# Performance work log

Measured on AMD Instinct MI355X. Metric: run time of the kernel, lower is better.

The kernel has to match this reference:

```python
import jax, jax.numpy as jnp
import numpy as np

B, T, D, E, L, MAXP, PRED, TOPK = 128, 2048, 256, 32, 8, 168, 168, 2
INIT_STD = 0.02


def setup_inputs() -> dict:
    key = jax.random.key(0)
    ks = jax.random.split(key, 18)
    n = jax.random.normal
    s = INIT_STD
    inp = {
        "ctx_embed": n(ks[0], (B, T, D), jnp.float32),
        "query_experts": n(ks[1], (E, MAXP, D), jnp.float32) * s,
        "query_pos": n(ks[2], (MAXP, D), jnp.float32) * s,
        "len_emb": n(ks[3], (MAXP + 1, D), jnp.float32),  # nn.Embedding table
        "latents": n(ks[4], (L, D), jnp.float32) * s,
        "w_lat_q": n(ks[5], (D, D), jnp.float32) / np.sqrt(D),
        "w_ctx_k": n(ks[6], (D, D), jnp.float32) / np.sqrt(D),
        "w_ctx_v": n(ks[7], (D, D), jnp.float32) / np.sqrt(D),
        "w_lat_out": n(ks[8], (D, D), jnp.float32) / np.sqrt(D),
        "w_step_q": n(ks[9], (D, D), jnp.float32) / np.sqrt(D),
        "w_lat_k": n(ks[10], (D, D), jnp.float32) / np.sqrt(D),
        "w_lat_v": n(ks[11], (D, D), jnp.float32) / np.sqrt(D),
        "w_step_out": n(ks[12], (D, D), jnp.float32) / np.sqrt(D),
        "gate_w1": n(ks[13], (2 * D, D), jnp.float32) / np.sqrt(2 * D),
        "gate_b1": jnp.zeros((D,), jnp.float32),
        "gate_w2": n(ks[14], (D, E), jnp.float32) / np.sqrt(D),
        "gate_b2": jnp.zeros((E,), jnp.float32),
        "pred_len": PRED,
    }
    return inp


def _sdpa_1head(q, k, v):
    # q: [B,Q,D], k/v: [B,K,D]; single-head scaled dot-product attention
    scale = jnp.asarray(q.shape[-1], q.dtype) ** -0.5
    attn = jax.nn.softmax(jnp.einsum('bqd,bkd->bqk', q, k) * scale, axis=-1)
    return jnp.einsum('bqk,bkd->bqd', attn, v)


def reference(ctx_embed, query_experts, query_pos, len_emb, latents,
              w_lat_q, w_ctx_k, w_ctx_v, w_lat_out,
              w_step_q, w_lat_k, w_lat_v, w_step_out,
              gate_w1, gate_b1, gate_w2, gate_b2, pred_len):
    Bb, Tt, Dd = ctx_embed.shape
    P = pred_len

    # step base: positional queries + pred-length embedding
    pos = query_pos[:P][None]                      # [1,P,D]
    len_vec = len_emb[P][None, None]               # [1,1,D]
    step_base = jnp.broadcast_to(pos + len_vec, (Bb, P, Dd))

    # latent <- context cross-attention
    lat = jnp.broadcast_to(latents[None], (Bb, latents.shape[0], Dd))
    q1 = lat @ w_lat_q
    k1 = ctx_embed @ w_ctx_k
    v1 = ctx_embed @ w_ctx_v
    lat_ctx = _sdpa_1head(q1, k1, v1) @ w_lat_out  # [B,L,D]

    # step <- latent cross-attention
    q2 = step_base @ w_step_q
    k2 = lat_ctx @ w_lat_k
    v2 = lat_ctx @ w_lat_v
    step_ctx = _sdpa_1head(q2, k2, v2) @ w_step_out  # [B,P,D]

    # gating MLP over [step_base, step_ctx]
    gate_inp = jnp.concatenate([step_base, step_ctx], axis=-1)  # [B,P,2D]
    h = jax.nn.gelu(gate_inp @ gate_w1 + gate_b1, approximate=False)
    logits = h @ gate_w2 + gate_b2                               # [B,P,E]

    # top-k masking + softmax (keep top-k logits, others -> -inf)
    topv = jax.lax.top_k(logits, TOPK)[0]
    kth = topv[..., -1:]
    masked = jnp.where(logits >= kth, logits, -jnp.inf)
    weights = jax.nn.softmax(masked, axis=-1)                    # [B,P,E]

    # mixture of expert queries (einsum avoids [B,P,E,D] intermediate)
    queries = jnp.einsum('bpe,epd->bpd', weights, query_experts[:, :P, :])
    return queries
```

## Files before the change

### kernel.cpp

```cpp
#include <hip/hip_runtime.h>
#include <math.h>

#define NB 128
#define NT 2048
#define ND 256
#define NE 32
#define NL 8
#define NP 168
#define SCL 0.0625f

#define OFF_QK   0
#define OFF_LATQ 2048
#define OFF_WVO  4096
#define OFF_WSO1 69632
#define OFF_WVW  135168
#define OFF_G0   200704
#define OFF_Q2S  243712
#define OFF_AV   286720
#define OFF_DEN  2383872
#define OFF_K2   2392064
#define OFF_VW   2654208

typedef __attribute__((ext_vector_type(8))) short short8b;
typedef __attribute__((ext_vector_type(4))) float f32x4;

static __device__ __forceinline__ unsigned short f2bf(float f){
  unsigned u = __float_as_uint(f);
  u += 0x7fffu + ((u >> 16) & 1u);
  return (unsigned short)(u >> 16);
}

static __device__ __forceinline__ short8b pack8(float4 lo, float4 hi){
  short8b r;
  r[0]=(short)f2bf(lo.x); r[1]=(short)f2bf(lo.y); r[2]=(short)f2bf(lo.z); r[3]=(short)f2bf(lo.w);
  r[4]=(short)f2bf(hi.x); r[5]=(short)f2bf(hi.y); r[6]=(short)f2bf(hi.z); r[7]=(short)f2bf(hi.w);
  return r;
}

__global__ __launch_bounds__(256) void pre1(const float* __restrict__ latents,
    const float* __restrict__ wlq, const float* __restrict__ wcv,
    const float* __restrict__ wlo, const float* __restrict__ wso,
    const float* __restrict__ gw1, const float* __restrict__ gb1,
    const float* __restrict__ qpos, const float* __restrict__ lemb,
    const float* __restrict__ wsq, float* __restrict__ ws)
{
  int bid = blockIdx.x, tid = threadIdx.x;
  if (bid < 256){
    const float* a = wcv + bid*ND;
    float acc = 0.f;
    #pragma unroll 8
    for (int k=0;k<ND;k++) acc += a[k]*wlo[k*ND+tid];
    ws[OFF_WVO + bid*ND + tid] = acc;
  } else if (bid < 512){
    int i = bid-256;
    const float* a = wso + i*ND;
    float acc = 0.f;
    #pragma unroll 8
    for (int k=0;k<ND;k++) acc += a[k]*gw1[(ND+k)*ND+tid];
    ws[OFF_WSO1 + i*ND + tid] = acc;
  } else if (bid < 512+NP){
    int p = bid-512;
    float ag = gb1[tid], aq = 0.f;
    #pragma unroll 4
    for (int j=0;j<ND;j++){
      float sb = qpos[p*ND+j] + lemb[NP*ND+j];
      ag += sb*gw1[j*ND+tid];
      aq += sb*wsq[j*ND+tid];
    }
    ws[OFF_G0  + p*ND + tid] = ag;
    ws[OFF_Q2S + p*ND + tid] = aq*SCL;
  } else {
    int l = bid-(512+NP);
    float acc = 0.f;
    #pragma unroll 8
    for (int m=0;m<ND;m++) acc += latents[l*ND+m]*wlq[m*ND+tid];
    ws[OFF_LATQ + l*ND + tid] = acc;
  }
}

__global__ __launch_bounds__(256) void pre2(const float* __restrict__ wck,
                                            const float* __restrict__ wlv,
                                            float* __restrict__ ws)
{
  int bid = blockIdx.x, tid = threadIdx.x;
  if (bid < 256){
    int d = bid;
    float wk = wck[d*ND + tid];
    float part[NL];
    #pragma unroll
    for (int l=0;l<NL;l++) part[l] = ws[OFF_LATQ + l*ND + tid]*wk;
    #pragma unroll
    for (int m=1;m<64;m<<=1){
      #pragma unroll
      for (int l=0;l<NL;l++) part[l] += __shfl_xor(part[l], m);
    }
    __shared__ float red[4][NL];
    if ((tid&63)==0){
      #pragma unroll
      for (int l=0;l<NL;l++) red[tid>>6][l] = part[l];
    }
    __syncthreads();
    if (tid < NL){
      float s = red[0][tid]+red[1][tid]+red[2][tid]+red[3][tid];
      ws[OFF_QK + tid*ND + d] = s*SCL;
    }
  } else {
    int dd = bid - 256;
    const float* a = wlv + dd*ND;
    float acc = 0.f;
    #pragma unroll 8
    for (int k=0;k<ND;k++) acc += a[k]*ws[OFF_WSO1 + k*ND + tid];
    ws[OFF_WVW + dd*ND + tid] = acc;
  }
}

__global__ __launch_bounds__(256,1) void kA(const float* __restrict__ ctx, float* __restrict__ ws)
{
  __shared__ float buf[2][64*256];
  __shared__ float efull[256*8];

  int bid = blockIdx.x;
  int b = bid >> 3, sp = bid & 7;
  int tid = threadIdx.x;
  int wv = tid >> 6, lane = tid & 63;
  int c = lane & 15, g = lane >> 4;
  int dq = lane;
  const int T0 = sp*256;

  short8b afrag[8];
  if (c < NL){
    const float* qk = ws + OFF_QK + c*ND + g*8;
    #pragma unroll
    for (int kk=0;kk<8;kk++){
      float4 lo = *(const float4*)(qk + kk*32);
      float4 hi = *(const float4*)(qk + kk*32 + 4);
      afrag[kk] = pack8(lo, hi);
    }
  } else {
    short8b z;
    #pragma unroll
    for (int j=0;j<8;j++) z[j] = 0;
    #pragma unroll
    for (int kk=0;kk<8;kk++) afrag[kk] = z;
  }

  float av[8][4];
  #pragma unroll
  for (int l=0;l<8;l++){
    #pragma unroll
    for (int j=0;j<4;j++) av[l][j] = 0.f;
  }

  int rr = wv*16 + c, r7 = rr & 7;

  int lofs[8];
  #pragma unroll
  for (int j=0;j<8;j++) lofs[j] = (lane ^ j) << 2;

  const float* g0 = ctx + ((size_t)(b*NT + T0 + wv*16))*ND;

#define STAGE(PBUF, GPTR) do{                                                     \
    _Pragma("unroll")                                                             \
    for (int i_=0;i_<16;i_++){                                                    \
      __builtin_amdgcn_global_load_lds(                                           \
          (const __attribute__((address_space(1))) void*)((GPTR) + i_*ND + lofs[i_&7]), \
          (__attribute__((address_space(3))) void*)((PBUF) + (wv*16+i_)*256), 16, 0, 0); \
    }                                                                             \
  }while(0)

  float* pc = &buf[0][0];
  float* pn = &buf[1][0];
  STAGE(pc, g0);

  #pragma unroll 1
  for (int sub=0; sub<4; ++sub){
    asm volatile("s_waitcnt lgkmcnt(0)" ::: "memory");
    __builtin_amdgcn_sched_barrier(0);
    if (sub < 3){
      STAGE(pn, g0 + (size_t)(sub+1)*64*ND);
      asm volatile("s_waitcnt vmcnt(16)" ::: "memory");
    } else {
      asm volatile("s_waitcnt vmcnt(0)" ::: "memory");
    }
    __builtin_amdgcn_sched_barrier(0);

    f32x4 acc = {0.f,0.f,0.f,0.f};
    #pragma unroll
    for (int kk=0;kk<8;kk++){
      int sA = 2*g + 8*kk;
      float4 lo = *(const float4*)(pc + rr*256 + (((sA  ) ^ r7)<<2));
      float4 hi = *(const float4*)(pc + rr*256 + (((sA+1) ^ r7)<<2));
      acc = __builtin_amdgcn_mfma_f32_16x16x32_bf16(afrag[kk], pack8(lo,hi), acc, 0, 0, 0);
    }
    if (g < 2){
      float4 ev = make_float4(__expf(acc[0]),__expf(acc[1]),__expf(acc[2]),__expf(acc[3]));
      *(float4*)&efull[(sub*64 + rr)*8 + g*4] = ev;
    }
    asm volatile("s_waitcnt lgkmcnt(0)" ::: "memory");
    __builtin_amdgcn_sched_barrier(0);

    #pragma unroll
    for (int i=0;i<16;i++){
      int tl = wv*16 + i;
      float4 c4 = *(const float4*)(pc + tl*256 + ((dq ^ (tl&7))<<2));
      const float* ep = efull + (sub*64 + tl)*8;
      float4 e0 = *(const float4*)ep;
      float4 e1 = *(const float4*)(ep+4);
      float e8[8];
      e8[0]=e0.x; e8[1]=e0.y; e8[2]=e0.z; e8[3]=e0.w;
      e8[4]=e1.x; e8[5]=e1.y; e8[6]=e1.z; e8[7]=e1.w;
      #pragma unroll
      for (int l=0;l<8;l++){
        av[l][0] += e8[l]*c4.x;
        av[l][1] += e8[l]*c4.y;
        av[l][2] += e8[l]*c4.z;
        av[l][3] += e8[l]*c4.w;
      }
    }
    float* t_ = pc; pc = pn; pn = t_;
  }
#undef STAGE

  __syncthreads();

  float* red = &buf[0][0];
  #pragma unroll
  for (int l=0;l<8;l++)
    *(float4*)(red + (((l*4 + wv)*64 + dq)<<2)) = make_float4(av[l][0],av[l][1],av[l][2],av[l][3]);

  if (wv == 0){
    float dpart[8];
    #pragma unroll
    for (int l=0;l<8;l++) dpart[l] = 0.f;
    #pragma unroll
    for (int q=0;q<4;q++){
      const float* ep = efull + (q*64 + lane)*8;
      float4 e0 = *(const float4*)ep;
      float4 e1 = *(const float4*)(ep+4);
      dpart[0]+=e0.x; dpart[1]+=e0.y; dpart[2]+=e0.z; dpart[3]+=e0.w;
      dpart[4]+=e1.x; dpart[5]+=e1.y; dpart[6]+=e1.z; dpart[7]+=e1.w;
    }
    #pragma unroll
    for (int m=1;m<64;m<<=1){
      #pragma unroll
      for (int l=0;l<8;l++) dpart[l] += __shfl_xor(dpart[l], m);
    }
    if (lane == 0){
      #pragma unroll
      for (int l=0;l<8;l++) ws[OFF_DEN + bid*8 + l] = dpart[l];
    }
  }
  __syncthreads();

  #pragma unroll
  for (int rep=0; rep<2; ++rep){
    int lidx = tid + rep*256;
    int l = lidx >> 6, d2 = lidx & 63;
    float4 s0 = *(const float4*)(red + (((l*4 + 0)*64 + d2)<<2));
    float4 s1 = *(const float4*)(red + (((l*4 + 1)*64 + d2)<<2));
    float4 s2 = *(const float4*)(red + (((l*4 + 2)*64 + d2)<<2));
    float4 s3 = *(const float4*)(red + (((l*4 + 3)*64 + d2)<<2));
    float4 o;
    o.x = s0.x+s1.x+s2.x+s3.x;
    o.y = s0.y+s1.y+s2.y+s3.y;
    o.z = s0.z+s1.z+s2.z+s3.z;
    o.w = s0.w+s1.w+s2.w+s3.w;
    *(float4*)&ws[OFF_AV + ((size_t)(bid*8 + l))*ND + d2*4] = o;
  }
}

__global__ __launch_bounds__(256) void kB1(const float* __restrict__ wlk,
                                           float* __restrict__ ws)
{
  int bid = blockIdx.x;
  int b = bid >> 1, half = bid & 1;
  int d = threadIdx.x;
  __shared__ float avnT[256][8];
  __shared__ float latT[256][8];

  float dent[8];
  #pragma unroll
  for (int l=0;l<8;l++){
    float s = 0.f;
    #pragma unroll
    for (int sp=0;sp<8;sp++) s += ws[OFF_DEN + (b*8+sp)*8 + l];
    dent[l] = s;
  }
  float av8[8];
  #pragma unroll
  for (int l=0;l<8;l++){
    float s = 0.f;
    #pragma unroll
    for (int sp=0;sp<8;sp++) s += ws[OFF_AV + ((size_t)((b*8+sp)*8 + l))*ND + d];
    av8[l] = s / dent[l];
  }
  *(float4*)&avnT[d][0] = make_float4(av8[0],av8[1],av8[2],av8[3]);
  *(float4*)&avnT[d][4] = make_float4(av8[4],av8[5],av8[6],av8[7]);
  __syncthreads();

  float lc[8];
  #pragma unroll
  for (int l=0;l<8;l++) lc[l] = 0.f;
  #pragma unroll 8
  for (int dd=0;dd<ND;dd++){
    float w = ws[OFF_WVO + dd*ND + d];
    float4 a0 = *(const float4*)&avnT[dd][0];
    float4 a1 = *(const float4*)&avnT[dd][4];
    lc[0]+=a0.x*w; lc[1]+=a0.y*w; lc[2]+=a0.z*w; lc[3]+=a0.w*w;
    lc[4]+=a1.x*w; lc[5]+=a1.y*w; lc[6]+=a1.z*w; lc[7]+=a1.w*w;
  }
  *(float4*)&latT[d][0] = make_float4(lc[0],lc[1],lc[2],lc[3]);
  *(float4*)&latT[d][4] = make_float4(lc[4],lc[5],lc[6],lc[7]);
  __syncthreads();

  const float* w3 = half ? (ws + OFF_WVW) : wlk;
  float o8[8];
  #pragma unroll
  for (int l=0;l<8;l++) o8[l] = 0.f;
  #pragma unroll 8
  for (int dd=0;dd<ND;dd++){
    float w = w3[dd*ND + d];
    float4 a0 = *(const float4*)&latT[dd][0];
    float4 a1 = *(const float4*)&latT[dd][4];
    o8[0]+=a0.x*w; o8[1]+=a0.y*w; o8[2]+=a0.z*w; o8[3]+=a0.w*w;
    o8[4]+=a1.x*w; o8[5]+=a1.y*w; o8[6]+=a1.z*w; o8[7]+=a1.w*w;
  }
  size_t obase = (half ? OFF_VW : OFF_K2) + (size_t)b*8*ND + d;
  #pragma unroll
  for (int l=0;l<8;l++) ws[obase + l*ND] = o8[l];
}

__global__ __launch_bounds__(256) void kB2(const float* __restrict__ ws,
    const float* __restrict__ gw2, const float* __restrict__ gb2,
    const float* __restrict__ qe, float* __restrict__ out)
{
  int bid = blockIdx.x;
  int b = bid / 6, p0 = (bid % 6)*28;
  int tid = threadIdx.x;

  __shared__ float q2h[28][260];
  __shared__ float k2s[8][260];
  __shared__ float vws[8][260];
  __shared__ float wexp[28][8];
  __shared__ float lg[28][33];
  __shared__ float4 sel[28];

  #pragma unroll
  for (int i=0;i<7;i++){
    int idx = tid + i*256;
    int r = idx >> 6, c4 = idx & 63;
    *(float4*)&q2h[r][c4*4] = *(const float4*)&ws[OFF_Q2S + (p0+r)*ND + c4*4];
  }
  #pragma unroll
  for (int i=0;i<2;i++){
    int idx = tid + i*256;
    int l = idx >> 6, c4 = idx & 63;
    *(float4*)&k2s[l][c4*4] = *(const float4*)&ws[OFF_K2 + (b*8+l)*ND + c4*4];
    *(float4*)&vws[l][c4*4] = *(const float4*)&ws[OFF_VW + (b*8+l)*ND + c4*4];
  }
  __syncthreads();

  {
    int pp = tid >> 3, l1 = tid & 7;
    if (pp < 28){
      float s2 = 0.f;
      #pragma unroll 8
      for (int i=0;i<64;i++){
        float4 qa = *(const float4*)&q2h[pp][4*i];
        float4 kb = *(const float4*)&k2s[l1][4*i];
        s2 += qa.x*kb.x + qa.y*kb.y + qa.z*kb.z + qa.w*kb.w;
      }
      float e2 = __expf(s2);
      float den = e2;
      den += __shfl_xor(den,1); den += __shfl_xor(den,2); den += __shfl_xor(den,4);
      wexp[pp][l1] = e2/den;
    }
  }
  __syncthreads();

  {
    float vcol[8];
    #pragma unroll
    for (int l=0;l<8;l++) vcol[l] = vws[l][tid];
    #pragma unroll 4
    for (int p=0;p<28;p++){
      float4 w0 = *(const float4*)&wexp[p][0];
      float4 w1v = *(const float4*)&wexp[p][4];
      float x = ws[OFF_G0 + (p0+p)*ND + tid]
              + w0.x*vcol[0]+w0.y*vcol[1]+w0.z*vcol[2]+w0.w*vcol[3]
              + w1v.x*vcol[4]+w1v.y*vcol[5]+w1v.z*vcol[6]+w1v.w*vcol[7];
      q2h[p][tid] = 0.5f*x*(1.f+erff(x*0.70710678118654752f));
    }
  }
  __syncthreads();

  {
    int e = tid & 31, pq = tid >> 5;
    if (pq < 7){
      float b2v = gb2[e];
      float a0=b2v, a1=b2v, a2=b2v, a3=b2v;
      for (int cc=0;cc<ND;cc+=4){
        float w20 = gw2[(cc+0)*NE + e];
        float w21 = gw2[(cc+1)*NE + e];
        float w22 = gw2[(cc+2)*NE + e];
        float w23 = gw2[(cc+3)*NE + e];
        float4 h0 = *(const float4*)&q2h[pq*4+0][cc];
        float4 h1 = *(const float4*)&q2h[pq*4+1][cc];
        float4 h2 = *(const float4*)&q2h[pq*4+2][cc];
        float4 h3 = *(const float4*)&q2h[pq*4+3][cc];
        a0 += h0.x*w20 + h0.y*w21 + h0.z*w22 + h0.w*w23;
        a1 += h1.x*w20 + h1.y*w21 + h1.z*w22 + h1.w*w23;
        a2 += h2.x*w20 + h2.y*w21 + h2.z*w22 + h2.w*w23;
        a3 += h3.x*w20 + h3.y*w21 + h3.z*w22 + h3.w*w23;
      }
      lg[pq*4+0][e] = a0;
      lg[pq*4+1][e] = a1;
      lg[pq*4+2][e] = a2;
      lg[pq*4+3][e] = a3;
    }
  }
  __syncthreads();

  if (tid < 28){
    float m1 = -1e30f, m2 = -1e30f;
    int e1 = 0, ee2 = 0;
    for (int e3=0;e3<NE;e3++){
      float v = lg[tid][e3];
      if (v > m1){ m2 = m1; ee2 = e1; m1 = v; e1 = e3; }
      else if (v > m2){ m2 = v; ee2 = e3; }
    }
    float z = __expf(m2 - m1);
    float inv = 1.f/(1.f+z);
    sel[tid] = make_float4(__int_as_float(e1), __int_as_float(ee2), inv, z*inv);
  }
  __syncthreads();

  for (int p=0;p<28;p++){
    float4 s = sel[p];
    int e1 = __float_as_int(s.x), ee2 = __float_as_int(s.y);
    float q1v = qe[((size_t)e1*NP + (p0+p))*ND + tid];
    float q2v = qe[((size_t)ee2*NP + (p0+p))*ND + tid];
    out[((size_t)b*NP + (p0+p))*ND + tid] = s.z*q1v + s.w*q2v;
  }
}

extern "C" void kernel_launch(void* const* d_in, const int* in_sizes, int n_in,
                              void* d_out, int out_size, void* d_ws, size_t ws_size,
                              hipStream_t stream)
{
  const float* ctx  = (const float*)d_in[0];
  const float* qe   = (const float*)d_in[1];
  const float* qpos = (const float*)d_in[2];
  const float* lemb = (const float*)d_in[3];
  const float* lat  = (const float*)d_in[4];
  const float* wlq  = (const float*)d_in[5];
  const float* wck  = (const float*)d_in[6];
  const float* wcv  = (const float*)d_in[7];
  const float* wlo  = (const float*)d_in[8];
  const float* wsq  = (const float*)d_in[9];
  const float* wlk  = (const float*)d_in[10];
  const float* wlv  = (const float*)d_in[11];
  const float* wso  = (const float*)d_in[12];
  const float* gw1  = (const float*)d_in[13];
  const float* gb1  = (const float*)d_in[14];
  const float* gw2  = (const float*)d_in[15];
  const float* gb2  = (const float*)d_in[16];
  float* out = (float*)d_out;
  float* ws  = (float*)d_ws;

  pre1<<<512+NP+NL, 256, 0, stream>>>(lat, wlq, wcv, wlo, wso, gw1, gb1, qpos, lemb, wsq, ws);
  pre2<<<512, 256, 0, stream>>>(wck, wlv, ws);
  kA  <<<NB*8, 256, 0, stream>>>(ctx, ws);
  kB1 <<<NB*2, 256, 0, stream>>>(wlk, ws);
  kB2 <<<NB*6, 256, 0, stream>>>(ws, gw2, gb2, qe, out);
}
```

Before: 164.2 us.

## Merge precompute kernels and make context-attention blocks persistent over many tiles

The two weight-precompute kernels become one launch. Each block recomputes its intermediate products locally, either through a shared-memory temporary or by reassociating the latent-query/key product, so pre2 no longer waits on pre1. The context-attention kernel now launches 256 persistent blocks, each streaming 16 tiles of 64 rows with double buffering. It writes per-wave partial attention sums and denominators instead of reducing in shared memory across waves. kB1 merges its two halves into one block per batch that sums 32 partials each, which cuts launches and block startup cost but enlarges the workspace partial traffic and halves parallelism in kB1.

```diff
diff --git a/kernel.cpp b/kernel.cpp
--- a/kernel.cpp
+++ b/kernel.cpp
@@ -10,16 +10,14 @@
 #define SCL 0.0625f
 
 #define OFF_QK   0
-#define OFF_LATQ 2048
 #define OFF_WVO  4096
-#define OFF_WSO1 69632
-#define OFF_WVW  135168
-#define OFF_G0   200704
-#define OFF_Q2S  243712
-#define OFF_AV   286720
-#define OFF_DEN  2383872
-#define OFF_K2   2392064
-#define OFF_VW   2654208
+#define OFF_WVW  69632
+#define OFF_G0   135168
+#define OFF_Q2S  178176
+#define OFF_AV   221184
+#define OFF_DEN  8609792
+#define OFF_K2   8642560
+#define OFF_VW   8904704
 
 typedef __attribute__((ext_vector_type(8))) short short8b;
 typedef __attribute__((ext_vector_type(4))) float f32x4;
@@ -37,9 +35,10 @@
   return r;
 }
 
-__global__ __launch_bounds__(256) void pre1(const float* __restrict__ latents,
-    const float* __restrict__ wlq, const float* __restrict__ wcv,
-    const float* __restrict__ wlo, const float* __restrict__ wso,
+__global__ __launch_bounds__(256) void preA(const float* __restrict__ latents,
+    const float* __restrict__ wlq, const float* __restrict__ wck,
+    const float* __restrict__ wcv, const float* __restrict__ wlo,
+    const float* __restrict__ wlv, const float* __restrict__ wso,
     const float* __restrict__ gw1, const float* __restrict__ gb1,
     const float* __restrict__ qpos, const float* __restrict__ lemb,
     const float* __restrict__ wsq, float* __restrict__ ws)
@@ -51,15 +50,8 @@
     #pragma unroll 8
     for (int k=0;k<ND;k++) acc += a[k]*wlo[k*ND+tid];
     ws[OFF_WVO + bid*ND + tid] = acc;
-  } else if (bid < 512){
-    int i = bid-256;
-    const float* a = wso + i*ND;
-    float acc = 0.f;
-    #pragma unroll 8
-    for (int k=0;k<ND;k++) acc += a[k]*gw1[(ND+k)*ND+tid];
-    ws[OFF_WSO1 + i*ND + tid] = acc;
-  } else if (bid < 512+NP){
-    int p = bid-512;
+  } else if (bid < 256+NP){
+    int p = bid-256;
     float ag = gb1[tid], aq = 0.f;
     #pragma unroll 4
     for (int j=0;j<ND;j++){
@@ -69,32 +61,28 @@
     }
     ws[OFF_G0  + p*ND + tid] = ag;
     ws[OFF_Q2S + p*ND + tid] = aq*SCL;
-  } else {
-    int l = bid-(512+NP);
-    float acc = 0.f;
+  } else if (bid < 256+NP+256){
+    int d = bid-(256+NP);
+    __shared__ float ck[ND];
+    __shared__ float red[4][NL];
+    ck[tid] = wck[d*ND + tid];
+    __syncthreads();
+    const float* wrow = wlq + tid*ND;
+    float macc = 0.f;
     #pragma unroll 8
-    for (int m=0;m<ND;m++) acc += latents[l*ND+m]*wlq[m*ND+tid];
-    ws[OFF_LATQ + l*ND + tid] = acc;
-  }
-}
-
-__global__ __launch_bounds__(256) void pre2(const float* __restrict__ wck,
-                                            const float* __restrict__ wlv,
-                                            float* __restrict__ ws)
-{
-  int bid = blockIdx.x, tid = threadIdx.x;
-  if (bid < 256){
-    int d = bid;
-    float wk = wck[d*ND + tid];
+    for (int k4=0;k4<64;k4++){
+      float4 w4 = *(const float4*)(wrow + k4*4);
+      float4 c4 = *(const float4*)(ck + k4*4);
+      macc += w4.x*c4.x + w4.y*c4.y + w4.z*c4.z + w4.w*c4.w;
+    }
     float part[NL];
     #pragma unroll
-    for (int l=0;l<NL;l++) part[l] = ws[OFF_LATQ + l*ND + tid]*wk;
+    for (int l=0;l<NL;l++) part[l] = latents[l*ND + tid]*macc;
     #pragma unroll
     for (int m=1;m<64;m<<=1){
       #pragma unroll
       for (int l=0;l<NL;l++) part[l] += __shfl_xor(part[l], m);
     }
-    __shared__ float red[4][NL];
     if ((tid&63)==0){
       #pragma unroll
       for (int l=0;l<NL;l++) red[tid>>6][l] = part[l];
@@ -105,11 +93,18 @@
       ws[OFF_QK + tid*ND + d] = s*SCL;
     }
   } else {
-    int dd = bid - 256;
+    int dd = bid-(256+NP+256);
+    __shared__ float tmp[ND];
     const float* a = wlv + dd*ND;
+    float t = 0.f;
+    #pragma unroll 8
+    for (int k=0;k<ND;k++) t += a[k]*wso[k*ND+tid];
+    tmp[tid] = t;
+    __syncthreads();
+    const float* gw1b = gw1 + (size_t)ND*ND;
     float acc = 0.f;
     #pragma unroll 8
-    for (int k=0;k<ND;k++) acc += a[k]*ws[OFF_WSO1 + k*ND + tid];
+    for (int m=0;m<ND;m++) acc += tmp[m]*gw1b[m*ND+tid];
     ws[OFF_WVW + dd*ND + tid] = acc;
   }
 }
@@ -120,12 +115,11 @@
   __shared__ float efull[256*8];
 
   int bid = blockIdx.x;
-  int b = bid >> 3, sp = bid & 7;
   int tid = threadIdx.x;
   int wv = tid >> 6, lane = tid & 63;
   int c = lane & 15, g = lane >> 4;
   int dq = lane;
-  const int T0 = sp*256;
+  int rr = wv*16 + c, r7 = rr & 7;
 
   short8b afrag[8];
   if (c < NL){
@@ -145,19 +139,19 @@
   }
 
   float av[8][4];
+  float den8[8];
   #pragma unroll
   for (int l=0;l<8;l++){
+    den8[l] = 0.f;
     #pragma unroll
     for (int j=0;j<4;j++) av[l][j] = 0.f;
   }
 
-  int rr = wv*16 + c, r7 = rr & 7;
-
   int lofs[8];
   #pragma unroll
   for (int j=0;j<8;j++) lofs[j] = (lane ^ j) << 2;
 
-  const float* g0 = ctx + ((size_t)(b*NT + T0 + wv*16))*ND;
+  const float* gw = ctx + ((size_t)bid*1024 + wv*16)*ND;
 
 #define STAGE(PBUF, GPTR) do{                                                     \
     _Pragma("unroll")                                                             \
@@ -168,16 +162,17 @@
     }                                                                             \
   }while(0)
 
-  float* pc = &buf[0][0];
-  float* pn = &buf[1][0];
-  STAGE(pc, g0);
+  STAGE(&buf[0][0], gw);
 
   #pragma unroll 1
-  for (int sub=0; sub<4; ++sub){
+  for (int s=0; s<16; ++s){
+    float* pc = &buf[s&1][0];
+    float* pn = &buf[(s&1)^1][0];
+    int sub = s & 3;
     asm volatile("s_waitcnt lgkmcnt(0)" ::: "memory");
     __builtin_amdgcn_sched_barrier(0);
-    if (sub < 3){
-      STAGE(pn, g0 + (size_t)(sub+1)*64*ND);
+    if (s < 15){
+      STAGE(pn, gw + (size_t)(s+1)*64*ND);
       asm volatile("s_waitcnt vmcnt(16)" ::: "memory");
     } else {
       asm volatile("s_waitcnt vmcnt(0)" ::: "memory");
@@ -215,85 +210,60 @@
         av[l][1] += e8[l]*c4.y;
         av[l][2] += e8[l]*c4.z;
         av[l][3] += e8[l]*c4.w;
+        den8[l]  += e8[l];
       }
     }
-    float* t_ = pc; pc = pn; pn = t_;
+
+    if (sub == 3){
+      int cid = bid*4 + (s>>2);
+      int pi  = cid*4 + wv;
+      #pragma unroll
+      for (int l=0;l<8;l++){
+        *(float4*)&ws[OFF_AV + ((size_t)pi*8 + l)*ND + dq*4] =
+            make_float4(av[l][0],av[l][1],av[l][2],av[l][3]);
+        av[l][0]=0.f; av[l][1]=0.f; av[l][2]=0.f; av[l][3]=0.f;
+      }
+      if (lane == 0){
+        *(float4*)&ws[OFF_DEN + pi*8    ] = make_float4(den8[0],den8[1],den8[2],den8[3]);
+        *(float4*)&ws[OFF_DEN + pi*8 + 4] = make_float4(den8[4],den8[5],den8[6],den8[7]);
+      }
+      #pragma unroll
+      for (int l=0;l<8;l++) den8[l] = 0.f;
+    }
   }
 #undef STAGE
-
-  __syncthreads();
-
-  float* red = &buf[0][0];
-  #pragma unroll
-  for (int l=0;l<8;l++)
-    *(float4*)(red + (((l*4 + wv)*64 + dq)<<2)) = make_float4(av[l][0],av[l][1],av[l][2],av[l][3]);
-
-  if (wv == 0){
-    float dpart[8];
-    #pragma unroll
-    for (int l=0;l<8;l++) dpart[l] = 0.f;
-    #pragma unroll
-    for (int q=0;q<4;q++){
-      const float* ep = efull + (q*64 + lane)*8;
-      float4 e0 = *(const float4*)ep;
-      float4 e1 = *(const float4*)(ep+4);
-      dpart[0]+=e0.x; dpart[1]+=e0.y; dpart[2]+=e0.z; dpart[3]+=e0.w;
-      dpart[4]+=e1.x; dpart[5]+=e1.y; dpart[6]+=e1.z; dpart[7]+=e1.w;
-    }
-    #pragma unroll
-    for (int m=1;m<64;m<<=1){
-      #pragma unroll
-      for (int l=0;l<8;l++) dpart[l] += __shfl_xor(dpart[l], m);
-    }
-    if (lane == 0){
-      #pragma unroll
-      for (int l=0;l<8;l++) ws[OFF_DEN + bid*8 + l] = dpart[l];
-    }
-  }
-  __syncthreads();
-
-  #pragma unroll
-  for (int rep=0; rep<2; ++rep){
-    int lidx = tid + rep*256;
-    int l = lidx >> 6, d2 = lidx & 63;
-    float4 s0 = *(const float4*)(red + (((l*4 + 0)*64 + d2)<<2));
-    float4 s1 = *(const float4*)(red + (((l*4 + 1)*64 + d2)<<2));
-    float4 s2 = *(const float4*)(red + (((l*4 + 2)*64 + d2)<<2));
-    float4 s3 = *(const float4*)(red + (((l*4 + 3)*64 + d2)<<2));
-    float4 o;
-    o.x = s0.x+s1.x+s2.x+s3.x;
-    o.y = s0.y+s1.y+s2.y+s3.y;
-    o.z = s0.z+s1.z+s2.z+s3.z;
-    o.w = s0.w+s1.w+s2.w+s3.w;
-    *(float4*)&ws[OFF_AV + ((size_t)(bid*8 + l))*ND + d2*4] = o;
-  }
 }
 
 __global__ __launch_bounds__(256) void kB1(const float* __restrict__ wlk,
                                            float* __restrict__ ws)
 {
-  int bid = blockIdx.x;
-  int b = bid >> 1, half = bid & 1;
+  int b = blockIdx.x;
   int d = threadIdx.x;
   __shared__ float avnT[256][8];
   __shared__ float latT[256][8];
 
   float dent[8];
   #pragma unroll
-  for (int l=0;l<8;l++){
-    float s = 0.f;
-    #pragma unroll
-    for (int sp=0;sp<8;sp++) s += ws[OFF_DEN + (b*8+sp)*8 + l];
-    dent[l] = s;
+  for (int l=0;l<8;l++) dent[l] = 0.f;
+  #pragma unroll 4
+  for (int j=0;j<32;j++){
+    const float* dp = ws + OFF_DEN + (size_t)(b*32+j)*8;
+    float4 d0 = *(const float4*)dp;
+    float4 d1 = *(const float4*)(dp+4);
+    dent[0]+=d0.x; dent[1]+=d0.y; dent[2]+=d0.z; dent[3]+=d0.w;
+    dent[4]+=d1.x; dent[5]+=d1.y; dent[6]+=d1.z; dent[7]+=d1.w;
   }
   float av8[8];
   #pragma unroll
-  for (int l=0;l<8;l++){
-    float s = 0.f;
-    #pragma unroll
-    for (int sp=0;sp<8;sp++) s += ws[OFF_AV + ((size_t)((b*8+sp)*8 + l))*ND + d];
-    av8[l] = s / dent[l];
-  }
+  for (int l=0;l<8;l++) av8[l] = 0.f;
+  #pragma unroll 2
+  for (int j=0;j<32;j++){
+    size_t base = OFF_AV + ((size_t)(b*32+j))*8*ND + d;
+    #pragma unroll
+    for (int l=0;l<8;l++) av8[l] += ws[base + (size_t)l*ND];
+  }
+  #pragma unroll
+  for (int l=0;l<8;l++) av8[l] /= dent[l];
   *(float4*)&avnT[d][0] = make_float4(av8[0],av8[1],av8[2],av8[3]);
   *(float4*)&avnT[d][4] = make_float4(av8[4],av8[5],av8[6],av8[7]);
   __syncthreads();
@@ -313,21 +283,25 @@
   *(float4*)&latT[d][4] = make_float4(lc[4],lc[5],lc[6],lc[7]);
   __syncthreads();
 
-  const float* w3 = half ? (ws + OFF_WVW) : wlk;
-  float o8[8];
-  #pragma unroll
-  for (int l=0;l<8;l++) o8[l] = 0.f;
+  float k2a[8], vwa[8];
+  #pragma unroll
+  for (int l=0;l<8;l++){ k2a[l]=0.f; vwa[l]=0.f; }
   #pragma unroll 8
   for (int dd=0;dd<ND;dd++){
-    float w = w3[dd*ND + d];
+    float wk = wlk[dd*ND + d];
+    float wvv = ws[OFF_WVW + dd*ND + d];
     float4 a0 = *(const float4*)&latT[dd][0];
     float4 a1 = *(const float4*)&latT[dd][4];
-    o8[0]+=a0.x*w; o8[1]+=a0.y*w; o8[2]+=a0.z*w; o8[3]+=a0.w*w;
-    o8[4]+=a1.x*w; o8[5]+=a1.y*w; o8[6]+=a1.z*w; o8[7]+=a1.w*w;
-  }
-  size_t obase = (half ? OFF_VW : OFF_K2) + (size_t)b*8*ND + d;
-  #pragma unroll
-  for (int l=0;l<8;l++) ws[obase + l*ND] = o8[l];
+    k2a[0]+=a0.x*wk; k2a[1]+=a0.y*wk; k2a[2]+=a0.z*wk; k2a[3]+=a0.w*wk;
+    k2a[4]+=a1.x*wk; k2a[5]+=a1.y*wk; k2a[6]+=a1.z*wk; k2a[7]+=a1.w*wk;
+    vwa[0]+=a0.x*wvv; vwa[1]+=a0.y*wvv; vwa[2]+=a0.z*wvv; vwa[3]+=a0.w*wvv;
+    vwa[4]+=a1.x*wvv; vwa[5]+=a1.y*wvv; vwa[6]+=a1.z*wvv; vwa[7]+=a1.w*wvv;
+  }
+  #pragma unroll
+  for (int l=0;l<8;l++){
+    ws[OFF_K2 + (size_t)b*8*ND + l*ND + d] = k2a[l];
+    ws[OFF_VW + (size_t)b*8*ND + l*ND + d] = vwa[l];
+  }
 }
 
 __global__ __launch_bounds__(256) void kB2(const float* __restrict__ ws,
@@ -355,8 +329,8 @@
   for (int i=0;i<2;i++){
     int idx = tid + i*256;
     int l = idx >> 6, c4 = idx & 63;
-    *(float4*)&k2s[l][c4*4] = *(const float4*)&ws[OFF_K2 + (b*8+l)*ND + c4*4];
-    *(float4*)&vws[l][c4*4] = *(const float4*)&ws[OFF_VW + (b*8+l)*ND + c4*4];
+    *(float4*)&k2s[l][c4*4] = *(const float4*)&ws[OFF_K2 + (size_t)(b*8+l)*ND + c4*4];
+    *(float4*)&vws[l][c4*4] = *(const float4*)&ws[OFF_VW + (size_t)(b*8+l)*ND + c4*4];
   }
   __syncthreads();
 
@@ -468,9 +442,9 @@
   float* out = (float*)d_out;
   float* ws  = (float*)d_ws;
 
-  pre1<<<512+NP+NL, 256, 0, stream>>>(lat, wlq, wcv, wlo, wso, gw1, gb1, qpos, lemb, wsq, ws);
-  pre2<<<512, 256, 0, stream>>>(wck, wlv, ws);
-  kA  <<<NB*8, 256, 0, stream>>>(ctx, ws);
-  kB1 <<<NB*2, 256, 0, stream>>>(wlk, ws);
+  preA<<<256+NP+256+256, 256, 0, stream>>>(lat, wlq, wck, wcv, wlo, wlv, wso,
+                                           gw1, gb1, qpos, lemb, wsq, ws);
+  kA  <<<256, 256, 0, stream>>>(ctx, ws);
+  kB1 <<<NB, 256, 0, stream>>>(wlk, ws);
   kB2 <<<NB*6, 256, 0, stream>>>(ws, gw2, gb2, qe, out);
 }
```

Result: no change. 165.1 us (+0.5%).
